# Kernel optimization log

Hardware: AMD Instinct MI355X
Metric: run time of the kernel (lower is better)

The kernel has to match this reference:

```python
import jax, jax.numpy as jnp
import numpy as np

B, D, U = 8192, 1024, 1024

def setup_inputs() -> dict:
    key = jax.random.key(0)
    ks = jax.random.split(key, 20)
    s = 0.02
    inp = {
        'x': jax.random.normal(ks[0], (B, D), jnp.float32),
        'h': jax.random.normal(ks[1], (B, U), jnp.float32),
        'c': jax.random.normal(ks[2], (B, U), jnp.float32),
        'W_i': jax.random.normal(ks[3], (D, U), jnp.float32) * s,
        'W_f': jax.random.normal(ks[4], (D, U), jnp.float32) * s,
        'W_c': jax.random.normal(ks[5], (D, U), jnp.float32) * s,
        'W_o': jax.random.normal(ks[6], (D, U), jnp.float32) * s,
        'U_i': jax.random.normal(ks[7], (U, U), jnp.float32) * s,
        'U_f': jax.random.normal(ks[8], (U, U), jnp.float32) * s,
        'U_c': jax.random.normal(ks[9], (U, U), jnp.float32) * s,
        'U_o': jax.random.normal(ks[10], (U, U), jnp.float32) * s,
        'V_i': jnp.ones((U,), jnp.float32),
        'V_f': jnp.ones((U,), jnp.float32),
        'V_o': jnp.ones((U,), jnp.float32),
        'b_i': jnp.zeros((U,), jnp.float32),
        'b_f': jnp.ones((U,), jnp.float32),
        'b_c': jnp.zeros((U,), jnp.float32),
        'b_o': jnp.zeros((U,), jnp.float32),
    }
    return inp


def reference(x, h, c, W_i, W_f, W_c, W_o, U_i, U_f, U_c, U_o,
              V_i, V_f, V_o, b_i, b_f, b_c, b_o):
    # Fuse the 4 input and 4 recurrent projections into two GEMMs.
    W = jnp.concatenate([W_i, W_f, W_c, W_o], axis=1)   # [D, 4U]
    Uw = jnp.concatenate([U_i, U_f, U_c, U_o], axis=1)  # [U, 4U]
    b = jnp.concatenate([b_i, b_f, b_c, b_o])           # [4U]
    z = x @ W + h @ Uw + b                               # [B, 4U]
    zi, zf, zc, zo = jnp.split(z, 4, axis=1)
    i_t = jax.nn.sigmoid(zi + V_i * c)
    f_t = jax.nn.sigmoid(zf + V_f * c)
    c_tilde = jnp.tanh(zc)
    c_t = f_t * c + i_t * c_tilde
    o_t = jax.nn.sigmoid(zo + V_o * c_t)
    h_t = o_t * jnp.tanh(c_t)
    return (h_t, c_t)
```

## Files before the change

kernel.cpp:

```cpp
#include <hip/hip_runtime.h>
#include <hip/hip_bf16.h>
#include <stdint.h>


#define MM 8192
#define KK 2048
#define NN 4096
#define BM 128
#define BN 128
#define BK 64

typedef __attribute__((ext_vector_type(8))) __bf16 bf16x8;
typedef __attribute__((ext_vector_type(4))) float floatx4;
typedef __attribute__((ext_vector_type(8))) unsigned short ushort8_t;

__device__ __forceinline__ unsigned short f2bf(float f) {
    unsigned int u = __float_as_uint(f);
    u += 0x7FFF + ((u >> 16) & 1);
    return (unsigned short)(u >> 16);
}

__device__ __forceinline__ float fast_sigmoid(float x) {
    return 1.0f / (1.0f + __expf(-x));
}

__device__ __forceinline__ float fast_tanh(float x) {
    return 2.0f / (1.0f + __expf(-2.0f * x)) - 1.0f;
}

__device__ __forceinline__ void async_copy16(const void* g, void* l) {
    __builtin_amdgcn_global_load_lds(
        (const __attribute__((address_space(1))) void*)g,
        (__attribute__((address_space(3))) void*)l,
        16, 0, 0);
}

__global__ void pack_all(const float* __restrict__ x, const float* __restrict__ h,
                         const float* __restrict__ Wi, const float* __restrict__ Wf,
                         const float* __restrict__ Wc, const float* __restrict__ Wo,
                         const float* __restrict__ Ui, const float* __restrict__ Uf,
                         const float* __restrict__ Uc, const float* __restrict__ Uo,
                         unsigned short* __restrict__ A,
                         unsigned short* __restrict__ Wt) {
    __shared__ float tile[64][68];
    int blk = blockIdx.x;
    int tid = threadIdx.x;
    if (blk >= 2048) {
        int t = (blk - 2048) * 256 + tid;
        long base = (long)t * 8;
        int row = (int)(base >> 11);
        int col = (int)(base & 2047);
        const float* src = (col < 1024) ? (x + (long)row * 1024 + col)
                                        : (h + (long)row * 1024 + (col - 1024));
        float4 v0 = *(const float4*)src;
        float4 v1 = *(const float4*)(src + 4);
        ushort8_t o;
        o[0] = f2bf(v0.x); o[1] = f2bf(v0.y); o[2] = f2bf(v0.z); o[3] = f2bf(v0.w);
        o[4] = f2bf(v1.x); o[5] = f2bf(v1.y); o[6] = f2bf(v1.z); o[7] = f2bf(v1.w);
        *(ushort8_t*)(A + base) = o;
        return;
    }
    int z = blk >> 8;
    int rem = blk & 255;
    const float* src;
    switch (z) {
        case 0: src = Wi; break; case 1: src = Wf; break;
        case 2: src = Wc; break; case 3: src = Wo; break;
        case 4: src = Ui; break; case 5: src = Uf; break;
        case 6: src = Uc; break; default: src = Uo; break;
    }
    int g = z & 3;
    int koff = (z >= 4) ? 1024 : 0;
    int d0 = (rem >> 4) * 64;
    int u0 = (rem & 15) * 64;

    int li = tid >> 4;
    int lj = (tid & 15) * 4;
#pragma unroll
    for (int p = 0; p < 4; ++p) {
        int i = p * 16 + li;
        float4 v = *(const float4*)(src + (long)(d0 + i) * 1024 + u0 + lj);
        *(float4*)&tile[i][lj] = v;
    }
    __syncthreads();
    int sj = tid >> 3;
    int sd = (tid & 7) * 8;
#pragma unroll
    for (int t = 0; t < 2; ++t) {
        int j = t * 32 + sj;
        ushort8_t o;
#pragma unroll
        for (int e = 0; e < 8; ++e) o[e] = f2bf(tile[sd + e][j]);
        long orow = (long)((u0 + j) * 4 + g);
        *(ushort8_t*)(Wt + orow * 2048 + koff + d0 + sd) = o;
    }
}

__global__ __launch_bounds__(256) void lstm_gemm(
    const unsigned short* __restrict__ A,
    const unsigned short* __restrict__ Wt,
    const float* __restrict__ c_in,
    const float* __restrict__ Vi, const float* __restrict__ Vf, const float* __restrict__ Vo,
    const float* __restrict__ bi_p, const float* __restrict__ bf_p,
    const float* __restrict__ bc_p, const float* __restrict__ bo_p,
    float* __restrict__ out) {
    __shared__ __align__(16) char smem[32768];
    unsigned short* As = (unsigned short*)smem;
    unsigned short* Bs = (unsigned short*)(smem + 16384);

    int tid = threadIdx.x;
    int wave = tid >> 6;
    int lane = tid & 63;
    int wm = wave >> 1, wn = wave & 1;

    int id = blockIdx.x;
    int bx = id & 63;
    int by = id >> 6;
    int rm0 = bx * BM;
    int cn0 = by * BN;

    int r_l = lane >> 3;
    int kc = ((lane & 7) ^ r_l) * 8;
    int voff = (wave * 32 + r_l) * 2048 + kc;
    const unsigned short* aP0 = A + (long)rm0 * 2048 + voff;
    const unsigned short* aP1 = aP0 + 8 * 2048;
    const unsigned short* aP2 = aP0 + 16 * 2048;
    const unsigned short* aP3 = aP0 + 24 * 2048;
    const unsigned short* bP0 = Wt + (long)cn0 * 2048 + voff;
    const unsigned short* bP1 = bP0 + 8 * 2048;
    const unsigned short* bP2 = bP0 + 16 * 2048;
    const unsigned short* bP3 = bP0 + 24 * 2048;
    char* ldsA = smem + wave * 4096;
    char* ldsB = smem + 16384 + wave * 4096;

    int fr = lane & 15;
    int fc = lane >> 4;
    int m7 = fr & 7;

    floatx4 acc[4][4];
#pragma unroll
    for (int i = 0; i < 4; ++i)
#pragma unroll
        for (int j = 0; j < 4; ++j) acc[i][j] = (floatx4)(0.0f);

#pragma unroll
    for (int kt = 0; kt < KK / BK; ++kt) {
        const int k0 = kt * BK;
        async_copy16(aP0 + k0, ldsA);
        async_copy16(aP1 + k0, ldsA + 1024);
        async_copy16(aP2 + k0, ldsA + 2048);
        async_copy16(aP3 + k0, ldsA + 3072);
        async_copy16(bP0 + k0, ldsB);
        async_copy16(bP1 + k0, ldsB + 1024);
        async_copy16(bP2 + k0, ldsB + 2048);
        async_copy16(bP3 + k0, ldsB + 3072);
        __syncthreads();

#pragma unroll
        for (int ks = 0; ks < 2; ++ks) {
            int sl = ((ks * 4 + fc) ^ m7) * 8;
            bf16x8 af[4], bfr[4];
#pragma unroll
            for (int mi = 0; mi < 4; ++mi)
                af[mi] = *(const bf16x8*)(As + (wm * 64 + mi * 16 + fr) * 64 + sl);
#pragma unroll
            for (int ni = 0; ni < 4; ++ni)
                bfr[ni] = *(const bf16x8*)(Bs + (wn * 64 + ni * 16 + fr) * 64 + sl);
#pragma unroll
            for (int mi = 0; mi < 4; ++mi)
#pragma unroll
                for (int ni = 0; ni < 4; ++ni)
                    acc[mi][ni] = __builtin_amdgcn_mfma_f32_16x16x32_bf16(
                        af[mi], bfr[ni], acc[mi][ni], 0, 0, 0);
        }
        __syncthreads();
    }

    float* zs = (float*)smem;
    int col = lane & 15;
    int q = lane >> 4;
    int u_b = tid & 31;
    int u_glob = by * 32 + u_b;
    float vVi = Vi[u_glob], vVf = Vf[u_glob], vVo = Vo[u_glob];
    float vbi = bi_p[u_glob], vbf = bf_p[u_glob], vbc = bc_p[u_glob], vbo = bo_p[u_glob];

#pragma unroll
    for (int mi = 0; mi < 4; ++mi) {
        if (mi) __syncthreads();
#pragma unroll
        for (int ni = 0; ni < 4; ++ni)
#pragma unroll
            for (int r = 0; r < 4; ++r)
                zs[(wm * 16 + q * 4 + r) * 132 + wn * 64 + ni * 16 + col] = acc[mi][ni][r];
        __syncthreads();
#pragma unroll
        for (int t = 0; t < 4; ++t) {
            int rowL = (tid >> 5) + t * 8;
            floatx4 z4 = *(const floatx4*)(zs + rowL * 132 + u_b * 4);
            long row_glob = rm0 + (rowL >> 4) * 64 + mi * 16 + (rowL & 15);
            float cv = c_in[row_glob * 1024 + u_glob];
            float i_t = fast_sigmoid(z4[0] + vbi + vVi * cv);
            float f_t = fast_sigmoid(z4[1] + vbf + vVf * cv);
            float ctl = fast_tanh(z4[2] + vbc);
            float c_t = f_t * cv + i_t * ctl;
            float o_t = fast_sigmoid(z4[3] + vbo + vVo * c_t);
            float h_t = o_t * fast_tanh(c_t);
            out[row_glob * 1024 + u_glob] = h_t;
            out[8388608 + row_glob * 1024 + u_glob] = c_t;
        }
    }
}

extern "C" void kernel_launch(void* const* d_in, const int* in_sizes, int n_in,
                              void* d_out, int out_size, void* d_ws, size_t ws_size,
                              hipStream_t stream) {
    const float* x  = (const float*)d_in[0];
    const float* h  = (const float*)d_in[1];
    const float* c  = (const float*)d_in[2];
    const float* Wi = (const float*)d_in[3];
    const float* Wf = (const float*)d_in[4];
    const float* Wc = (const float*)d_in[5];
    const float* Wo = (const float*)d_in[6];
    const float* Ui = (const float*)d_in[7];
    const float* Uf = (const float*)d_in[8];
    const float* Uc = (const float*)d_in[9];
    const float* Uo = (const float*)d_in[10];
    const float* Vi = (const float*)d_in[11];
    const float* Vf = (const float*)d_in[12];
    const float* Vo = (const float*)d_in[13];
    const float* bi = (const float*)d_in[14];
    const float* bf = (const float*)d_in[15];
    const float* bc = (const float*)d_in[16];
    const float* bo = (const float*)d_in[17];

    unsigned short* Abf = (unsigned short*)d_ws;
    unsigned short* Wt  = (unsigned short*)((char*)d_ws + 33554432);

    pack_all<<<dim3(10240), 256, 0, stream>>>(x, h, Wi, Wf, Wc, Wo,
                                              Ui, Uf, Uc, Uo, Abf, Wt);
    lstm_gemm<<<dim3(2048), 256, 0, stream>>>(Abf, Wt, c, Vi, Vf, Vo,
                                              bi, bf, bc, bo, (float*)d_out);
}
```

Baseline: 348.7 us.

## Fuse activation fp32-to-bf16 conversion into GEMM A-tile loads

Removes the separate pass that packs x and h into a bf16 workspace. The GEMM kernel now loads fp32 x/h directly, converts to bf16 in registers and writes swizzled LDS tiles, while B keeps async global-to-LDS copies. This saves a full write and re-read of the 32MB activation buffer. In exchange, A is fetched at fp32 width, each A tile is reloaded by every column block (64 times), and the synchronous loads plus conversion sit on the critical path with no async overlap.

Measured after the change: 472.0 us. 1.35x slower.

```diff
diff --git a/kernel.cpp b/kernel.cpp
--- a/kernel.cpp
+++ b/kernel.cpp
@@ -35,31 +35,14 @@
         16, 0, 0);
 }
 
-__global__ void pack_all(const float* __restrict__ x, const float* __restrict__ h,
-                         const float* __restrict__ Wi, const float* __restrict__ Wf,
-                         const float* __restrict__ Wc, const float* __restrict__ Wo,
-                         const float* __restrict__ Ui, const float* __restrict__ Uf,
-                         const float* __restrict__ Uc, const float* __restrict__ Uo,
-                         unsigned short* __restrict__ A,
-                         unsigned short* __restrict__ Wt) {
+__global__ void pack_w(const float* __restrict__ Wi, const float* __restrict__ Wf,
+                       const float* __restrict__ Wc, const float* __restrict__ Wo,
+                       const float* __restrict__ Ui, const float* __restrict__ Uf,
+                       const float* __restrict__ Uc, const float* __restrict__ Uo,
+                       unsigned short* __restrict__ Wt) {
     __shared__ float tile[64][68];
     int blk = blockIdx.x;
     int tid = threadIdx.x;
-    if (blk >= 2048) {
-        int t = (blk - 2048) * 256 + tid;
-        long base = (long)t * 8;
-        int row = (int)(base >> 11);
-        int col = (int)(base & 2047);
-        const float* src = (col < 1024) ? (x + (long)row * 1024 + col)
-                                        : (h + (long)row * 1024 + (col - 1024));
-        float4 v0 = *(const float4*)src;
-        float4 v1 = *(const float4*)(src + 4);
-        ushort8_t o;
-        o[0] = f2bf(v0.x); o[1] = f2bf(v0.y); o[2] = f2bf(v0.z); o[3] = f2bf(v0.w);
-        o[4] = f2bf(v1.x); o[5] = f2bf(v1.y); o[6] = f2bf(v1.z); o[7] = f2bf(v1.w);
-        *(ushort8_t*)(A + base) = o;
-        return;
-    }
     int z = blk >> 8;
     int rem = blk & 255;
     const float* src;
@@ -97,7 +80,8 @@
 }
 
 __global__ __launch_bounds__(256) void lstm_gemm(
-    const unsigned short* __restrict__ A,
+    const float* __restrict__ x,
+    const float* __restrict__ h,
     const unsigned short* __restrict__ Wt,
     const float* __restrict__ c_in,
     const float* __restrict__ Vi, const float* __restrict__ Vf, const float* __restrict__ Vo,
@@ -122,16 +106,18 @@
     int r_l = lane >> 3;
     int kc = ((lane & 7) ^ r_l) * 8;
     int voff = (wave * 32 + r_l) * 2048 + kc;
-    const unsigned short* aP0 = A + (long)rm0 * 2048 + voff;
-    const unsigned short* aP1 = aP0 + 8 * 2048;
-    const unsigned short* aP2 = aP0 + 16 * 2048;
-    const unsigned short* aP3 = aP0 + 24 * 2048;
     const unsigned short* bP0 = Wt + (long)cn0 * 2048 + voff;
     const unsigned short* bP1 = bP0 + 8 * 2048;
     const unsigned short* bP2 = bP0 + 16 * 2048;
     const unsigned short* bP3 = bP0 + 24 * 2048;
-    char* ldsA = smem + wave * 4096;
     char* ldsB = smem + 16384 + wave * 4096;
+
+    int ar = tid >> 1;
+    int hh = tid & 1;
+    const float* xBase = x + (long)(rm0 + ar) * 1024 + hh * 32;
+    const float* hBase = h + (long)(rm0 + ar) * 1024 + hh * 32;
+    unsigned short* aW = As + ar * 64;
+    int r7 = ar & 7;
 
     int fr = lane & 15;
     int fc = lane >> 4;
@@ -146,14 +132,26 @@
 #pragma unroll
     for (int kt = 0; kt < KK / BK; ++kt) {
         const int k0 = kt * BK;
-        async_copy16(aP0 + k0, ldsA);
-        async_copy16(aP1 + k0, ldsA + 1024);
-        async_copy16(aP2 + k0, ldsA + 2048);
-        async_copy16(aP3 + k0, ldsA + 3072);
         async_copy16(bP0 + k0, ldsB);
         async_copy16(bP1 + k0, ldsB + 1024);
         async_copy16(bP2 + k0, ldsB + 2048);
         async_copy16(bP3 + k0, ldsB + 3072);
+        {
+            const float* px = (kt < 16) ? (xBase + kt * 64) : (hBase + (kt - 16) * 64);
+            float4 va[8];
+#pragma unroll
+            for (int j = 0; j < 8; ++j) va[j] = *(const float4*)(px + j * 4);
+#pragma unroll
+            for (int i = 0; i < 4; ++i) {
+                bf16x8 o;
+                o[0] = (__bf16)va[2 * i].x;     o[1] = (__bf16)va[2 * i].y;
+                o[2] = (__bf16)va[2 * i].z;     o[3] = (__bf16)va[2 * i].w;
+                o[4] = (__bf16)va[2 * i + 1].x; o[5] = (__bf16)va[2 * i + 1].y;
+                o[6] = (__bf16)va[2 * i + 1].z; o[7] = (__bf16)va[2 * i + 1].w;
+                int slot = (hh * 4 + i) ^ r7;
+                *(bf16x8*)(aW + slot * 8) = o;
+            }
+        }
         __syncthreads();
 
 #pragma unroll
@@ -233,11 +231,9 @@
     const float* bc = (const float*)d_in[16];
     const float* bo = (const float*)d_in[17];
 
-    unsigned short* Abf = (unsigned short*)d_ws;
-    unsigned short* Wt  = (unsigned short*)((char*)d_ws + 33554432);
-
-    pack_all<<<dim3(10240), 256, 0, stream>>>(x, h, Wi, Wf, Wc, Wo,
-                                              Ui, Uf, Uc, Uo, Abf, Wt);
-    lstm_gemm<<<dim3(2048), 256, 0, stream>>>(Abf, Wt, c, Vi, Vf, Vo,
+    unsigned short* Wt = (unsigned short*)d_ws;
+
+    pack_w<<<dim3(2048), 256, 0, stream>>>(Wi, Wf, Wc, Wo, Ui, Uf, Uc, Uo, Wt);
+    lstm_gemm<<<dim3(2048), 256, 0, stream>>>(x, h, Wt, c, Vi, Vf, Vo,
                                               bi, bf, bc, bo, (float*)d_out);
 }
```
